# Kernel optimization log

Measured on AMD Instinct MI355X. Metric: run time of the kernel, lower is better.

Reference implementation:

```python
import jax, jax.numpy as jnp
import numpy as np

KER = 8

def _gelu(x):
    return jax.nn.gelu(x, approximate=False)

def _conv3x3(x, w, b):
    y = jax.lax.conv_general_dilated(x, w, (1, 1), 'SAME',
                                     dimension_numbers=('NCHW', 'OIHW', 'NCHW'))
    return y + b[None, :, None, None]

def _unfold(x):
    # F.unfold(kernel=8, stride=8): [B,C,H,W] -> [B, C*64, L], C-major then kh,kw
    B, C, H, W = x.shape
    Hb, Wb = H // KER, W // KER
    p = x.reshape(B, C, Hb, KER, Wb, KER).transpose(0, 1, 3, 5, 2, 4)
    return p.reshape(B, C * KER * KER, Hb * Wb)

def _fold(cols, H, W):
    # inverse of _unfold (non-overlapping patches)
    B, CK, L = cols.shape
    C = CK // (KER * KER)
    Hb, Wb = H // KER, W // KER
    p = cols.reshape(B, C, KER, KER, Hb, Wb).transpose(0, 1, 4, 2, 5, 3)
    return p.reshape(B, C, H, W)

def _bn(x, g, b, eps=1e-5):
    # train-mode BatchNorm1d on [B, C, L]: stats over (B, L) per channel
    m = x.mean(axis=(0, 2), keepdims=True)
    v = x.var(axis=(0, 2), keepdims=True)
    return (x - m) * jax.lax.rsqrt(v + eps) * g[None, :, None] + b[None, :, None]


def setup_inputs() -> dict:
    key = jax.random.key(0)
    ks = jax.random.split(key, 10)
    ind, d, hid = 64, 1024, 256
    f = lambda k, s: jax.random.normal(k, s, dtype=jnp.float32) * 0.02
    return {
        'feat': jax.random.normal(ks[0], (4, ind, 256, 256), dtype=jnp.float32),
        'w_enc': f(ks[1], (ind, ind, 3, 3)), 'b_enc': jnp.zeros((ind,), jnp.float32),
        'w_k': f(ks[2], (ind, ind, 3, 3)), 'b_k': jnp.zeros((ind,), jnp.float32),
        'w_v': f(ks[3], (ind, ind, 3, 3)), 'b_v': jnp.zeros((ind,), jnp.float32),
        'fcq_w': f(ks[4], (d, ind * KER * KER)), 'fcq_b': jnp.zeros((d,), jnp.float32),
        'fck_w': f(ks[5], (d, ind * KER * KER)), 'fck_b': jnp.zeros((d,), jnp.float32),
        'bnq_g': jnp.ones((d,), jnp.float32), 'bnq_b': jnp.zeros((d,), jnp.float32),
        'bnk_g': jnp.ones((d,), jnp.float32), 'bnk_b': jnp.zeros((d,), jnp.float32),
        'ff1_w': f(ks[6], (hid, ind)), 'ff1_b': jnp.zeros((hid,), jnp.float32),
        'ff2_w': f(ks[7], (ind, hid)), 'ff2_b': jnp.zeros((ind,), jnp.float32),
    }


def reference(feat, w_enc, b_enc, w_k, b_k, w_v, b_v,
              fcq_w, fcq_b, fck_w, fck_b, bnq_g, bnq_b, bnk_g, bnk_b,
              ff1_w, ff1_b, ff2_w, ff2_b):
    B, C, H, W = feat.shape
    fk = _gelu(_conv3x3(feat, w_k, b_k))
    fv = _gelu(_conv3x3(feat, w_v, b_v))
    refer = _gelu(_conv3x3(feat, w_enc, b_enc))
    q_un = _unfold(refer).transpose(0, 2, 1)   # [B, L, C*64]
    k_un = _unfold(fk).transpose(0, 2, 1)
    v_un = _unfold(fv).transpose(0, 2, 1)
    q = jnp.einsum('blc,dc->bld', q_un, fcq_w) + fcq_b
    q = _bn(q.transpose(0, 2, 1), bnq_g, bnq_b).transpose(0, 2, 1)  # [B, L, 1024]
    k = jnp.einsum('blc,dc->bld', k_un, fck_w) + fck_b
    k = _bn(k.transpose(0, 2, 1), bnk_g, bnk_b).transpose(0, 2, 1)
    scores = jnp.einsum('bld,bmd->blm', q, k) / jnp.sqrt(jnp.float32(q.shape[2]))
    attn = jax.nn.softmax(scores, axis=2)
    out = jnp.einsum('blm,bmc->blc', attn, v_un).transpose(0, 2, 1)  # [B, C*64, L]
    out = _fold(out, H, W)
    h = _gelu(jnp.einsum('bchw,oc->bohw', out, ff1_w) + ff1_b[None, :, None, None])
    h = _gelu(jnp.einsum('bchw,oc->bohw', h, ff2_w) + ff2_b[None, :, None, None])
    return h + feat
```

## Files before the change

kernel.cpp:

```cpp
#include <hip/hip_runtime.h>

typedef unsigned short u16;
typedef float f4 __attribute__((ext_vector_type(4)));
typedef float f32x4 __attribute__((ext_vector_type(4)));
typedef short bf16x8 __attribute__((ext_vector_type(8)));
typedef u16 u16x8 __attribute__((ext_vector_type(8)));
typedef u16 u16x4 __attribute__((ext_vector_type(4)));

__device__ __forceinline__ u16 f2bf(float f){
  unsigned u = __float_as_uint(f);
  u = (u + 0x7FFFu + ((u>>16)&1u)) >> 16;
  return (u16)u;
}
__device__ __forceinline__ float bf2f(u16 u){
  return __uint_as_float(((unsigned)u)<<16);
}
__device__ __forceinline__ float gelu_f(float x){
  float y = 1.5957691216057308f*(x + 0.044715f*x*x*x);
  y = fminf(y, 30.0f);
  float t = __expf(y);
  float r = __builtin_amdgcn_rcpf(t + 1.0f);
  return 0.5f*x*(1.0f + (t - 1.0f)*r);
}

typedef __attribute__((address_space(1))) const unsigned int as1_cuint;
typedef __attribute__((address_space(3))) unsigned int as3_uint;
__device__ __forceinline__ void gload_lds16(const void* g, void* l){
  __builtin_amdgcn_global_load_lds((as1_cuint*)g, (as3_uint*)l, 16, 0, 0);
}

__global__ __launch_bounds__(256) void to_nhwc(
    const float* __restrict__ F, u16* __restrict__ O)
{
  __shared__ float tile[64][65];
  const int t = threadIdx.x, b = blockIdx.y;
  const long px0 = (long)blockIdx.x*64;
  const float* Fb = F + (long)b*64*65536;
  #pragma unroll
  for (int i = 0; i < 4; ++i){
    const int ch = (t>>4) + i*16;
    const int pxo = (t&15)*4;
    f4 v = *(const f4*)&Fb[(long)ch*65536 + px0 + pxo];
    tile[ch][pxo]=v[0]; tile[ch][pxo+1]=v[1]; tile[ch][pxo+2]=v[2]; tile[ch][pxo+3]=v[3];
  }
  __syncthreads();
  const int px = t & 63, ch0 = (t>>6)*16;
  u16x8 o0, o1;
  #pragma unroll
  for (int j = 0; j < 8; ++j){ o0[j]=f2bf(tile[ch0+j][px]); o1[j]=f2bf(tile[ch0+8+j][px]); }
  u16* Ob = O + ((long)b*65536 + px0 + px)*64 + ch0;
  *(u16x8*)Ob = o0; *(u16x8*)(Ob+8) = o1;
}

__global__ __launch_bounds__(256) void wt_prep(
    const float* __restrict__ we, const float* __restrict__ wk,
    const float* __restrict__ wv, u16* __restrict__ Wt2)
{
  const int i = blockIdx.x*256 + threadIdx.x;
  const int cio = i & 31;
  const int t1 = i >> 5;
  const int n  = t1 % 192;
  const int t2 = t1 / 192;
  const int kc = t2 & 1, p = t2 >> 1;
  const int dy = p/3, dx = p - dy*3;
  const int ci = kc*32 + cio;
  const float* W = (n < 64) ? we : (n < 128) ? wk : wv;
  const int co = n & 63;
  Wt2[i] = f2bf(W[((co*64 + ci)*3 + dy)*3 + dx]);
}

__global__ __launch_bounds__(512,2) void conv_mfma(
    const u16* __restrict__ X, const u16* __restrict__ Wt2,
    const float* __restrict__ be, const float* __restrict__ bk, const float* __restrict__ bv,
    u16* __restrict__ Aq, u16* __restrict__ Ak, u16* __restrict__ Vl)
{
  __shared__ __align__(16) u16 smem[24576];
  const int t = threadIdx.x, lane = t & 63, wvi = t >> 6;
  const int bx = blockIdx.x, by = blockIdx.y, b = blockIdx.z;
  const int x0 = bx*16, y0 = by*8;
  const u16* Xb = X + (long)b*4194304;

  #pragma unroll
  for (int j = 0; j < 3; ++j){
    const int id = t + j*512;
    if (id < 1440){
      const int row = id / 144, rem = id - row*144, col = rem >> 3, ck = rem & 7;
      const int y = y0 - 1 + row, x = x0 - 1 + col;
      int4 v = {0,0,0,0};
      if ((unsigned)y < 256u && (unsigned)x < 256u)
        v = *(const int4*)(Xb + ((long)y*256 + x)*64 + ck*8);
      *(int4*)&smem[((row*18 + col)*8 + (ck ^ (col&7)))*8] = v;
    }
  }
  __syncthreads();

  const int wm4 = (wvi>>2)*4;
  const int wn  = (wvi&3)*48;
  const int fr = lane & 15, fo = lane >> 4;
  f32x4 acc[4][3] = {};

  #pragma unroll
  for (int dy = 0; dy < 3; ++dy)
  #pragma unroll
  for (int dx = 0; dx < 3; ++dx){
    const int p = dy*3 + dx;
    #pragma unroll
    for (int kc = 0; kc < 2; ++kc){
      bf16x8 af[4], bfv[3];
      const u16* wp = Wt2 + ((long)(p*2 + kc)*192 + wn + fr)*32 + fo*8;
      #pragma unroll
      for (int ni = 0; ni < 3; ++ni)
        bfv[ni] = *(const bf16x8*)(wp + ni*16*32);
      #pragma unroll
      for (int mi = 0; mi < 4; ++mi){
        const int row = wm4 + mi + dy;
        const int col = fr + dx;
        af[mi] = *(const bf16x8*)&smem[((row*18 + col)*8 + ((kc*4+fo) ^ (col&7)))*8];
      }
      #pragma unroll
      for (int mi = 0; mi < 4; ++mi)
        #pragma unroll
        for (int ni = 0; ni < 3; ++ni)
          acc[mi][ni] = __builtin_amdgcn_mfma_f32_16x16x32_bf16(af[mi], bfv[ni], acc[mi][ni], 0, 0, 0);
    }
  }
  __syncthreads();

  const int c0 = fo*4;
  const int lloc = c0 >> 3, kw0 = c0 & 7;
  #pragma unroll
  for (int ni = 0; ni < 3; ++ni){
    const int n = wn + ni*16 + fr;
    const int mat = n >> 6, co = n & 63;
    const float bias = (mat==0) ? be[co] : (mat==1) ? bk[co] : bv[co];
    #pragma unroll
    for (int mi = 0; mi < 4; ++mi){
      const int r = wm4 + mi;
      u16x4 o;
      #pragma unroll
      for (int rg = 0; rg < 4; ++rg) o[rg] = f2bf(gelu_f(acc[mi][ni][rg] + bias));
      const int e = ((mat*2 + lloc)*64 + co)*64 + ((r*8 + kw0) ^ ((co&7)<<3));
      *(u16x4*)&smem[e] = o;
    }
  }
  __syncthreads();

  const int l_lo = by*32 + bx*2;
  const int co_r = t >> 3, sw = (t&7) ^ (co_r&7);
  const int eoff = co_r*64 + sw*8;
  #pragma unroll
  for (int i = 0; i < 6; ++i){
    const int mat = i >> 1, ll = i & 1;
    u16x8 v = *(const u16x8*)&smem[(mat*2 + ll)*4096 + eoff];
    u16* dst = (mat==0 ? Aq : mat==1 ? Ak : Vl)
             + ((long)b*1024 + l_lo + ll)*4096 + t*8;
    *(u16x8*)dst = v;
  }
}

__global__ __launch_bounds__(256) void v_tr(
    const u16* __restrict__ S, u16* __restrict__ D)
{
  __shared__ u16 tl[64][72];
  const int t = threadIdx.x, b = blockIdx.z;
  const int ck0 = blockIdx.x*64, l0 = blockIdx.y*64;
  const u16* Sb = S + (long)b*4194304;
  u16* Db = D + (long)b*4194304;
  #pragma unroll
  for (int j = 0; j < 2; ++j){
    const int li = (t>>3) + j*32, cko = (t&7)*8;
    *(u16x8*)&tl[li][cko] = *(const u16x8*)(Sb + (long)(l0+li)*4096 + ck0 + cko);
  }
  __syncthreads();
  #pragma unroll
  for (int j = 0; j < 2; ++j){
    const int cki = (t>>3) + j*32, lo = (t&7)*8;
    u16x8 v;
    #pragma unroll
    for (int e = 0; e < 8; ++e) v[e] = tl[lo+e][cki];
    *(u16x8*)(Db + (long)(ck0+cki)*1024 + l0 + lo) = v;
  }
}

__device__ __forceinline__ void xcd_map(int gxl, int gyl, int n8l,
                                        int& bx, int& by, int& bz){
  const int s = blockIdx.x + (blockIdx.y<<gxl) + (blockIdx.z<<(gxl+gyl));
  const int orig = ((s & 7) << n8l) + (s >> 3);
  bx = orig & ((1<<gxl)-1);
  by = (orig >> gxl) & ((1<<gyl)-1);
  bz = orig >> (gxl+gyl);
}

template<int EPI>
__global__ __launch_bounds__(256,4) void gemm_bt64(
    const u16* __restrict__ A, long sA,
    const u16* __restrict__ B, long sB, const int zshB,
    void* __restrict__ Cv, long sC,
    const int M, const int N, const int K,
    float* __restrict__ bnstats,
    const int gxl, const int gyl, const int n8l)
{
  int bx, by, bI;
  xcd_map(gxl, gyl, n8l, bx, by, bI);
  const u16* Ab = A + (long)bI*sA;
  const u16* Bb = B + (long)(bI>>zshB)*sB;
  const int m0 = bx*64, n0 = by*128;
  __shared__ __align__(16) u16 As[4096];
  __shared__ __align__(16) u16 Bs[8192];
  const int t = threadIdx.x, lane = t & 63, wv = t >> 6;
  const int wm = (wv>>1)*32, wn = (wv&1)*64;
  const int fr = lane & 15, fo = lane >> 4;
  f32x4 acc[2][4] = {};
  const int ca  = wv*64 + lane;
  const int cb0 = wv*128 + lane, cb1 = cb0 + 64;
  const u16* Ag  = Ab + (long)(m0 + (ca >>2))*K + (ca &3)*8;
  const u16* Bg0 = Bb + (long)(n0 + (cb0>>2))*K + (cb0&3)*8;
  const u16* Bg1 = Bb + (long)(n0 + (cb1>>2))*K + (cb1&3)*8;
  gload_lds16(Ag,  &As[wv*512]);
  gload_lds16(Bg0, &Bs[wv*1024]);
  gload_lds16(Bg1, &Bs[wv*1024 + 512]);
  const int nk = K >> 5;
  int cur = 0;
  for (int ki = 0; ki < nk; ++ki){
    __syncthreads();
    if (ki + 1 < nk){
      const int k0 = (ki + 1) << 5;
      gload_lds16(Ag  + k0, &As[((cur^1)<<11) + wv*512]);
      gload_lds16(Bg0 + k0, &Bs[((cur^1)<<12) + wv*1024]);
      gload_lds16(Bg1 + k0, &Bs[((cur^1)<<12) + wv*1024 + 512]);
    }
    const int ra = cur << 11, rb = cur << 12;
    bf16x8 af[2], bfv[4];
    #pragma unroll
    for (int i = 0; i < 2; ++i)
      af[i]  = *(const bf16x8*)&As[ra + (wm + i*16 + fr)*32 + fo*8];
    #pragma unroll
    for (int i = 0; i < 4; ++i)
      bfv[i] = *(const bf16x8*)&Bs[rb + (wn + i*16 + fr)*32 + fo*8];
    #pragma unroll
    for (int mi = 0; mi < 2; ++mi)
      #pragma unroll
      for (int ni = 0; ni < 4; ++ni)
        acc[mi][ni] = __builtin_amdgcn_mfma_f32_16x16x32_bf16(af[mi], bfv[ni], acc[mi][ni], 0, 0, 0);
    cur ^= 1;
  }
  if (EPI == 0){
    float* Cf = (float*)Cv + (long)bI*sC;
    #pragma unroll
    for (int mi = 0; mi < 2; ++mi)
      #pragma unroll
      for (int ni = 0; ni < 4; ++ni){
        const int col = n0 + wn + ni*16 + fr;
        #pragma unroll
        for (int r = 0; r < 4; ++r){
          const int row = m0 + wm + mi*16 + fo*4 + r;
          Cf[(long)row*N + col] = acc[mi][ni][r];
        }
      }
  } else {
    u16* Cb = (u16*)Cv + (long)bI*sC;
    #pragma unroll
    for (int mi = 0; mi < 2; ++mi)
      #pragma unroll
      for (int ni = 0; ni < 4; ++ni){
        const int col = n0 + wn + ni*16 + fr;
        const int row0 = m0 + wm + mi*16 + fo*4;
        u16x4 o;
        #pragma unroll
        for (int r = 0; r < 4; ++r) o[r] = f2bf(acc[mi][ni][r]);
        *(u16x4*)&Cb[(long)col*M + row0] = o;
      }
    const int sel = bI >> 2;
    float* sums = bnstats + sel*2048;
    #pragma unroll
    for (int ni = 0; ni < 4; ++ni){
      float s = 0.f, q = 0.f;
      #pragma unroll
      for (int mi = 0; mi < 2; ++mi)
        #pragma unroll
        for (int r = 0; r < 4; ++r){
          const float v = acc[mi][ni][r];
          s += v; q += v*v;
        }
      s += __shfl_xor(s, 16); s += __shfl_xor(s, 32);
      q += __shfl_xor(q, 16); q += __shfl_xor(q, 32);
      if (fo == 0){
        const int col = n0 + wn + ni*16 + fr;
        atomicAdd(&sums[col], s);
        atomicAdd(&sums[1024 + col], q);
      }
    }
  }
}

__global__ __launch_bounds__(256,3) void gemm_bt(
    const u16* __restrict__ A, long sA,
    const u16* __restrict__ B, long sB,
    void* __restrict__ Cv,
    const int M, const int N, const int K,
    const int gxl, const int gyl, const int n8l)
{
  int bx, by, bI;
  xcd_map(gxl, gyl, n8l, bx, by, bI);
  const u16* Ab = A + (long)bI*sA;
  const u16* Bb = B + (long)bI*sB;
  const int m0 = bx*128, n0 = by*128;
  __shared__ __align__(16) u16 As[8192];
  __shared__ __align__(16) u16 Bs[8192];
  const int t = threadIdx.x, lane = t & 63, wv = t >> 6;
  const int wm = (wv>>1)*64, wn = (wv&1)*64;
  const int fr = lane & 15, fo = lane >> 4;
  f32x4 acc[4][4] = {};
  const int c0 = wv*128 + lane, c1 = c0 + 64;
  const u16* Ag0 = Ab + (long)(m0 + (c0>>2))*K + (c0&3)*8;
  const u16* Ag1 = Ab + (long)(m0 + (c1>>2))*K + (c1&3)*8;
  const u16* Bg0 = Bb + (long)(n0 + (c0>>2))*K + (c0&3)*8;
  const u16* Bg1 = Bb + (long)(n0 + (c1>>2))*K + (c1&3)*8;
  const int lo0 = wv*1024;
  gload_lds16(Ag0, &As[lo0]);
  gload_lds16(Ag1, &As[lo0 + 512]);
  gload_lds16(Bg0, &Bs[lo0]);
  gload_lds16(Bg1, &Bs[lo0 + 512]);
  const int nk = K >> 5;
  int cur = 0;
  for (int ki = 0; ki < nk; ++ki){
    __syncthreads();
    if (ki + 1 < nk){
      const int k0 = (ki + 1) << 5;
      const int so = ((cur^1) << 12) + lo0;
      gload_lds16(Ag0 + k0, &As[so]);
      gload_lds16(Ag1 + k0, &As[so + 512]);
      gload_lds16(Bg0 + k0, &Bs[so]);
      gload_lds16(Bg1 + k0, &Bs[so + 512]);
    }
    const int ro = cur << 12;
    bf16x8 af[4], bfv[4];
    #pragma unroll
    for (int i = 0; i < 4; ++i){
      af[i]  = *(const bf16x8*)&As[ro + (wm + i*16 + fr)*32 + fo*8];
      bfv[i] = *(const bf16x8*)&Bs[ro + (wn + i*16 + fr)*32 + fo*8];
    }
    #pragma unroll
    for (int mi = 0; mi < 4; ++mi)
      #pragma unroll
      for (int ni = 0; ni < 4; ++ni)
        acc[mi][ni] = __builtin_amdgcn_mfma_f32_16x16x32_bf16(af[mi], bfv[ni], acc[mi][ni], 0, 0, 0);
    cur ^= 1;
  }
  u16* O = (u16*)Cv;
  #pragma unroll
  for (int mi = 0; mi < 4; ++mi)
    #pragma unroll
    for (int ni = 0; ni < 4; ++ni){
      const int col = n0 + wn + ni*16 + fr;
      const int c = col >> 6, khh = (col>>3)&7, kww = col&7;
      #pragma unroll
      for (int r = 0; r < 4; ++r){
        const int row = m0 + wm + mi*16 + fo*4 + r;
        const int hb = row >> 5, wbb = row & 31;
        O[(((long)bI*65536 + (hb*8+khh)*256 + wbb*8 + kww)<<6) + c] = f2bf(acc[mi][ni][r]);
      }
    }
}

__global__ __launch_bounds__(256,3) void ff1_mfma(
    const u16* __restrict__ X, const u16* __restrict__ W1b,
    const float* __restrict__ B1, u16* __restrict__ H1)
{
  const int t = threadIdx.x, lane = t & 63, wv = t >> 6;
  const long m0 = (long)blockIdx.x*128 + (wv>>1)*64;
  const int n0 = blockIdx.y*128 + (wv&1)*64;
  const int fr = lane & 15, fo = lane >> 4;
  f32x4 acc[4][4] = {};
  #pragma unroll
  for (int k0 = 0; k0 < 64; k0 += 32){
    bf16x8 af[4], bfv[4];
    #pragma unroll
    for (int i = 0; i < 4; ++i){
      af[i]  = *(const bf16x8*)(X   + (m0 + i*16 + fr)*64 + k0 + fo*8);
      bfv[i] = *(const bf16x8*)(W1b + (long)(n0 + i*16 + fr)*64 + k0 + fo*8);
    }
    #pragma unroll
    for (int mi = 0; mi < 4; ++mi)
      #pragma unroll
      for (int ni = 0; ni < 4; ++ni)
        acc[mi][ni] = __builtin_amdgcn_mfma_f32_16x16x32_bf16(af[mi], bfv[ni], acc[mi][ni], 0, 0, 0);
  }
  #pragma unroll
  for (int ni = 0; ni < 4; ++ni){
    const int col = n0 + ni*16 + fr;
    const float bc = B1[col];
    #pragma unroll
    for (int mi = 0; mi < 4; ++mi){
      const long row = m0 + mi*16 + fo*4;
      #pragma unroll
      for (int r = 0; r < 4; ++r)
        H1[(row + r)*256 + col] = f2bf(gelu_f(acc[mi][ni][r] + bc));
    }
  }
}

__global__ __launch_bounds__(256,3) void ff2_mfma(
    const u16* __restrict__ H1, const u16* __restrict__ W2b,
    const float* __restrict__ B2, const float* __restrict__ F,
    float* __restrict__ OUT)
{
  const int t = threadIdx.x, lane = t & 63, wv = t >> 6;
  const long m0 = (long)blockIdx.x*256 + wv*64;
  const int fr = lane & 15, fo = lane >> 4;
  f32x4 acc[4][4] = {};
  for (int k0 = 0; k0 < 256; k0 += 32){
    bf16x8 af[4], bfv[4];
    #pragma unroll
    for (int i = 0; i < 4; ++i){
      af[i]  = *(const bf16x8*)(H1  + (m0 + i*16 + fr)*256 + k0 + fo*8);
      bfv[i] = *(const bf16x8*)(W2b + (long)(i*16 + fr)*256 + k0 + fo*8);
    }
    #pragma unroll
    for (int mi = 0; mi < 4; ++mi)
      #pragma unroll
      for (int ni = 0; ni < 4; ++ni)
        acc[mi][ni] = __builtin_amdgcn_mfma_f32_16x16x32_bf16(af[mi], bfv[ni], acc[mi][ni], 0, 0, 0);
  }
  #pragma unroll
  for (int ni = 0; ni < 4; ++ni){
    const int c = ni*16 + fr;
    const float bc = B2[c];
    #pragma unroll
    for (int mi = 0; mi < 4; ++mi){
      const long p = m0 + mi*16 + fo*4;
      const int b = (int)(p >> 16), pp = (int)(p & 65535);
      const long idx = ((long)(b*64 + c))*65536 + pp;
      const f4 fres = *(const f4*)&F[idx];
      f4 o;
      #pragma unroll
      for (int r = 0; r < 4; ++r) o[r] = gelu_f(acc[mi][ni][r] + bc) + fres[r];
      *(f4*)&OUT[idx] = o;
    }
  }
}

__global__ __launch_bounds__(256) void cvt_w(
    const float* __restrict__ Wq, const float* __restrict__ Wk,
    u16* __restrict__ Oq, u16* __restrict__ Ok)
{
  const long i = ((long)blockIdx.x*256 + threadIdx.x)*4;
  const float* s = blockIdx.y ? Wk : Wq;
  u16* d = blockIdx.y ? Ok : Oq;
  f4 v = *(const f4*)&s[i];
  u16x4 o; o[0]=f2bf(v[0]); o[1]=f2bf(v[1]); o[2]=f2bf(v[2]); o[3]=f2bf(v[3]);
  *(u16x4*)&d[i] = o;
}

__global__ __launch_bounds__(256) void cvt_ffw(
    const float* __restrict__ W1, const float* __restrict__ W2,
    u16* __restrict__ O1, u16* __restrict__ O2)
{
  const long i = ((long)blockIdx.x*256 + threadIdx.x)*4;
  const float* s = blockIdx.y ? W2 : W1;
  u16* d = blockIdx.y ? O2 : O1;
  f4 v = *(const f4*)&s[i];
  u16x4 o; o[0]=f2bf(v[0]); o[1]=f2bf(v[1]); o[2]=f2bf(v[2]); o[3]=f2bf(v[3]);
  *(u16x4*)&d[i] = o;
}

__global__ void bn_fin2(float* __restrict__ stats,
                        const float* __restrict__ gq, const float* __restrict__ bq,
                        const float* __restrict__ gk, const float* __restrict__ bk)
{
  const int sel = blockIdx.y;
  const int d = blockIdx.x*256 + threadIdx.x;
  if (d >= 1024) return;
  const float* sum   = stats + sel*2048;
  const float* sumsq = sum + 1024;
  const float* g    = sel ? gk : gq;
  const float* beta = sel ? bk : bq;
  const float m  = sum[d]   * (1.f/4096.f);
  const float vv = sumsq[d] * (1.f/4096.f) - m*m;
  const float sc = g[d] * rsqrtf(vv + 1e-5f);
  stats[4096 + sel*2048 + d]        = sc;
  stats[4096 + sel*2048 + 1024 + d] = beta[d] - m*sc;
}

__global__ __launch_bounds__(256) void bn_apply_t(
    const u16* __restrict__ QT, const float* __restrict__ stats,
    u16* __restrict__ Y)
{
  __shared__ u16 tl[64][72];
  const int t = threadIdx.x, zi = blockIdx.z;
  const int d0 = blockIdx.x*64, l0 = blockIdx.y*64;
  const int sel = zi >> 2;
  const u16* S = QT + (long)zi*1048576;
  u16* D = Y + (long)zi*1048576;
  const float* scp = stats + 4096 + sel*2048;
  const float* shp = scp + 1024;
  #pragma unroll
  for (int j = 0; j < 2; ++j){
    const int di = (t>>3) + j*32, lo = (t&7)*8;
    const int d = d0 + di;
    const float sc = scp[d], sh = shp[d];
    u16x8 v = *(const u16x8*)(S + (long)d*1024 + l0 + lo);
    u16x8 o;
    #pragma unroll
    for (int e = 0; e < 8; ++e) o[e] = f2bf(bf2f(v[e])*sc + sh);
    *(u16x8*)&tl[di][lo] = o;
  }
  __syncthreads();
  #pragma unroll
  for (int j = 0; j < 2; ++j){
    const int li = (t>>3) + j*32, dof = (t&7)*8;
    u16x8 v;
    #pragma unroll
    for (int e = 0; e < 8; ++e) v[e] = tl[dof+e][li];
    *(u16x8*)(D + (long)(l0+li)*1024 + d0 + dof) = v;
  }
}

__global__ __launch_bounds__(256) void softmax_k(
    const float* __restrict__ S, u16* __restrict__ P)
{
  const long row = blockIdx.x;
  const float* p = S + row*1024;
  const int t = threadIdx.x;
  f4 v = *(const f4*)&p[t*4];
  v *= 0.03125f;
  float mx = fmaxf(fmaxf(v[0],v[1]), fmaxf(v[2],v[3]));
  #pragma unroll
  for (int o = 1; o < 64; o <<= 1) mx = fmaxf(mx, __shfl_xor(mx, o));
  __shared__ float red[4], red2[4];
  if ((t & 63) == 0) red[t>>6] = mx;
  __syncthreads();
  mx = fmaxf(fmaxf(red[0],red[1]), fmaxf(red[2],red[3]));
  f4 e;
  e[0]=__expf(v[0]-mx); e[1]=__expf(v[1]-mx); e[2]=__expf(v[2]-mx); e[3]=__expf(v[3]-mx);
  float sm = e[0]+e[1]+e[2]+e[3];
  #pragma unroll
  for (int o = 1; o < 64; o <<= 1) sm += __shfl_xor(sm, o);
  if ((t & 63) == 0) red2[t>>6] = sm;
  __syncthreads();
  sm = red2[0]+red2[1]+red2[2]+red2[3];
  const float inv = 1.0f/sm;
  u16x4 o4; o4[0]=f2bf(e[0]*inv); o4[1]=f2bf(e[1]*inv); o4[2]=f2bf(e[2]*inv); o4[3]=f2bf(e[3]*inv);
  *(u16x4*)&P[row*1024 + t*4] = o4;
}

extern "C" void kernel_launch(void* const* d_in, const int* in_sizes, int n_in,
                              void* d_out, int out_size, void* d_ws, size_t ws_size,
                              hipStream_t stream)
{
  const float* feat  = (const float*)d_in[0];
  const float* w_enc = (const float*)d_in[1];
  const float* b_enc = (const float*)d_in[2];
  const float* w_k   = (const float*)d_in[3];
  const float* b_k   = (const float*)d_in[4];
  const float* w_v   = (const float*)d_in[5];
  const float* b_v   = (const float*)d_in[6];
  const float* fcq_w = (const float*)d_in[7];
  const float* fck_w = (const float*)d_in[9];
  const float* bnq_g = (const float*)d_in[11];
  const float* bnq_b = (const float*)d_in[12];
  const float* bnk_g = (const float*)d_in[13];
  const float* bnk_b = (const float*)d_in[14];
  const float* ff1w  = (const float*)d_in[15];
  const float* ff1b  = (const float*)d_in[16];
  const float* ff2w  = (const float*)d_in[17];
  const float* ff2b  = (const float*)d_in[18];

  char* ws = (char*)d_ws;
  u16*   Aq      = (u16*)  (ws);
  u16*   Ak      = (u16*)  (ws + (32ull<<20));
  u16*   Vc      = (u16*)  (ws + (64ull<<20));
  u16*   Wq      = (u16*)  (ws + (96ull<<20));
  u16*   Wk      = (u16*)  (ws + (104ull<<20));
  u16*   q_bf    = (u16*)  (ws + (112ull<<20));
  u16*   k_bf    = (u16*)  (ws + (120ull<<20));
  u16*   qk_rawT = (u16*)  (ws + (128ull<<20));
  float* scores  = (float*)(ws + (160ull<<20));
  u16*   attn    = (u16*)  (ws + (176ull<<20));
  u16*   out_nhwc= (u16*)  (ws + (184ull<<20));
  u16*   NX      = (u16*)  (ws + (128ull<<20));
  u16*   Vl      = (u16*)  (ws + (160ull<<20));
  u16*   Wt2     = (u16*)  (ws + (216ull<<20));
  float* stats   = (float*)(ws + (217ull<<20));
  u16*   W1b     = (u16*)  (ws + (218ull<<20));
  u16*   W2b     = (u16*)  (ws + (218ull<<20) + 65536);
  u16*   h1      = (u16*)  (ws);

  hipMemsetAsync(stats, 0, 4096*sizeof(float), stream);

  to_nhwc<<<dim3(1024,4), 256, 0, stream>>>(feat, NX);
  wt_prep<<<dim3(432), 256, 0, stream>>>(w_enc, w_k, w_v, Wt2);
  conv_mfma<<<dim3(16,32,4), 512, 0, stream>>>(NX, Wt2, b_enc, b_k, b_v, Aq, Ak, Vl);
  v_tr<<<dim3(64,16,4), 256, 0, stream>>>(Vl, Vc);
  cvt_w<<<dim3(4096,2), 256, 0, stream>>>(fcq_w, fck_w, Wq, Wk);
  cvt_ffw<<<dim3(16,2), 256, 0, stream>>>(ff1w, ff2w, W1b, W2b);

  gemm_bt64<2><<<dim3(16,8,8), 256, 0, stream>>>(Aq, 4194304, Wq, 4194304, 2,
                                                 qk_rawT, 1048576, 1024, 1024, 4096, stats,
                                                 4, 3, 7);

  bn_fin2<<<dim3(4,2), 256, 0, stream>>>(stats, bnq_g, bnq_b, bnk_g, bnk_b);
  bn_apply_t<<<dim3(16,16,8), 256, 0, stream>>>(qk_rawT, stats, q_bf);

  gemm_bt64<0><<<dim3(16,8,4), 256, 0, stream>>>(q_bf, 1048576, k_bf, 1048576, 0,
                                                 scores, 1048576, 1024, 1024, 1024, nullptr,
                                                 4, 3, 6);
  softmax_k<<<dim3(4096), 256, 0, stream>>>(scores, attn);

  gemm_bt<<<dim3(8,32,4), 256, 0, stream>>>(attn, 1048576, Vc, 4194304,
                                            out_nhwc, 1024, 4096, 1024,
                                            3, 5, 7);

  ff1_mfma<<<dim3(2048,2), 256, 0, stream>>>(out_nhwc, W1b, ff1b, h1);
  ff2_mfma<<<dim3(1024), 256, 0, stream>>>(h1, W2b, ff2b, feat, (float*)d_out);
}
```

Measured before the change: 526.2 us.

## Triple-buffer GEMM LDS staging with XOR swizzle and raised MFMA priority

Both bf16 GEMM kernels move from double to triple buffering of shared-memory tiles. Each iteration waits with a partial vmcnt and a raw s_barrier, so loads two k-steps ahead stay in flight while the current tile is computed. The global source column is XOR-swizzled to match the fragment read offsets, which reduces LDS bank conflicts. The MFMA block also runs at raised wave priority. The cost is 50% more LDS per block, which may lower occupancy, and the hand-written waitcnt/barrier asm is fragile.

```diff
diff --git a/kernel.cpp b/kernel.cpp
--- a/kernel.cpp
+++ b/kernel.cpp
@@ -27,6 +27,11 @@
 typedef __attribute__((address_space(3))) unsigned int as3_uint;
 __device__ __forceinline__ void gload_lds16(const void* g, void* l){
   __builtin_amdgcn_global_load_lds((as1_cuint*)g, (as3_uint*)l, 16, 0, 0);
+}
+
+__device__ __forceinline__ int gswz(int c){
+  const int r = c >> 2;
+  return (((c & 3) ^ ((r & 3) ^ ((r >> 2) & 3))) * 8);
 }
 
 __global__ __launch_bounds__(256) void to_nhwc(
@@ -205,45 +210,51 @@
   const u16* Ab = A + (long)bI*sA;
   const u16* Bb = B + (long)(bI>>zshB)*sB;
   const int m0 = bx*64, n0 = by*128;
-  __shared__ __align__(16) u16 As[4096];
-  __shared__ __align__(16) u16 Bs[8192];
+  __shared__ __align__(16) u16 As[6144];
+  __shared__ __align__(16) u16 Bs[12288];
   const int t = threadIdx.x, lane = t & 63, wv = t >> 6;
   const int wm = (wv>>1)*32, wn = (wv&1)*64;
   const int fr = lane & 15, fo = lane >> 4;
+  const int fosw = (fo ^ ((fr & 3) ^ ((fr >> 2) & 3))) * 8;
   f32x4 acc[2][4] = {};
   const int ca  = wv*64 + lane;
   const int cb0 = wv*128 + lane, cb1 = cb0 + 64;
-  const u16* Ag  = Ab + (long)(m0 + (ca >>2))*K + (ca &3)*8;
-  const u16* Bg0 = Bb + (long)(n0 + (cb0>>2))*K + (cb0&3)*8;
-  const u16* Bg1 = Bb + (long)(n0 + (cb1>>2))*K + (cb1&3)*8;
-  gload_lds16(Ag,  &As[wv*512]);
-  gload_lds16(Bg0, &Bs[wv*1024]);
-  gload_lds16(Bg1, &Bs[wv*1024 + 512]);
+  const u16* Ag  = Ab + (long)(m0 + (ca >>2))*K + gswz(ca);
+  const u16* Bg0 = Bb + (long)(n0 + (cb0>>2))*K + gswz(cb0);
+  const u16* Bg1 = Bb + (long)(n0 + (cb1>>2))*K + gswz(cb1);
+#define STAGE64(slot, kofs) { \
+    gload_lds16(Ag  + (kofs), &As[(slot)*2048 + wv*512]); \
+    gload_lds16(Bg0 + (kofs), &Bs[(slot)*4096 + wv*1024]); \
+    gload_lds16(Bg1 + (kofs), &Bs[(slot)*4096 + wv*1024 + 512]); }
+  STAGE64(0, 0)
+  STAGE64(1, 32)
   const int nk = K >> 5;
-  int cur = 0;
+  int sl = 0;
   for (int ki = 0; ki < nk; ++ki){
-    __syncthreads();
-    if (ki + 1 < nk){
-      const int k0 = (ki + 1) << 5;
-      gload_lds16(Ag  + k0, &As[((cur^1)<<11) + wv*512]);
-      gload_lds16(Bg0 + k0, &Bs[((cur^1)<<12) + wv*1024]);
-      gload_lds16(Bg1 + k0, &Bs[((cur^1)<<12) + wv*1024 + 512]);
-    }
-    const int ra = cur << 11, rb = cur << 12;
+    if (ki + 1 < nk) asm volatile("s_waitcnt vmcnt(3)\n\ts_barrier" ::: "memory");
+    else             asm volatile("s_waitcnt vmcnt(0)\n\ts_barrier" ::: "memory");
+    if (ki + 2 < nk){
+      const int s2 = (sl >= 1) ? sl - 1 : sl + 2;
+      STAGE64(s2, (ki + 2) << 5)
+    }
+    const int ra = sl*2048, rb = sl*4096;
     bf16x8 af[2], bfv[4];
     #pragma unroll
     for (int i = 0; i < 2; ++i)
-      af[i]  = *(const bf16x8*)&As[ra + (wm + i*16 + fr)*32 + fo*8];
+      af[i]  = *(const bf16x8*)&As[ra + (wm + i*16 + fr)*32 + fosw];
     #pragma unroll
     for (int i = 0; i < 4; ++i)
-      bfv[i] = *(const bf16x8*)&Bs[rb + (wn + i*16 + fr)*32 + fo*8];
+      bfv[i] = *(const bf16x8*)&Bs[rb + (wn + i*16 + fr)*32 + fosw];
+    __builtin_amdgcn_s_setprio(1);
     #pragma unroll
     for (int mi = 0; mi < 2; ++mi)
       #pragma unroll
       for (int ni = 0; ni < 4; ++ni)
         acc[mi][ni] = __builtin_amdgcn_mfma_f32_16x16x32_bf16(af[mi], bfv[ni], acc[mi][ni], 0, 0, 0);
-    cur ^= 1;
-  }
+    __builtin_amdgcn_s_setprio(0);
+    sl = (sl + 1 == 3) ? 0 : sl + 1;
+  }
+#undef STAGE64
   if (EPI == 0){
     float* Cf = (float*)Cv + (long)bI*sC;
     #pragma unroll
@@ -305,48 +316,53 @@
   const u16* Ab = A + (long)bI*sA;
   const u16* Bb = B + (long)bI*sB;
   const int m0 = bx*128, n0 = by*128;
-  __shared__ __align__(16) u16 As[8192];
-  __shared__ __align__(16) u16 Bs[8192];
+  __shared__ __align__(16) u16 As[12288];
+  __shared__ __align__(16) u16 Bs[12288];
   const int t = threadIdx.x, lane = t & 63, wv = t >> 6;
   const int wm = (wv>>1)*64, wn = (wv&1)*64;
   const int fr = lane & 15, fo = lane >> 4;
+  const int fosw = (fo ^ ((fr & 3) ^ ((fr >> 2) & 3))) * 8;
   f32x4 acc[4][4] = {};
   const int c0 = wv*128 + lane, c1 = c0 + 64;
-  const u16* Ag0 = Ab + (long)(m0 + (c0>>2))*K + (c0&3)*8;
-  const u16* Ag1 = Ab + (long)(m0 + (c1>>2))*K + (c1&3)*8;
-  const u16* Bg0 = Bb + (long)(n0 + (c0>>2))*K + (c0&3)*8;
-  const u16* Bg1 = Bb + (long)(n0 + (c1>>2))*K + (c1&3)*8;
-  const int lo0 = wv*1024;
-  gload_lds16(Ag0, &As[lo0]);
-  gload_lds16(Ag1, &As[lo0 + 512]);
-  gload_lds16(Bg0, &Bs[lo0]);
-  gload_lds16(Bg1, &Bs[lo0 + 512]);
+  const u16* Ag0 = Ab + (long)(m0 + (c0>>2))*K + gswz(c0);
+  const u16* Ag1 = Ab + (long)(m0 + (c1>>2))*K + gswz(c1);
+  const u16* Bg0 = Bb + (long)(n0 + (c0>>2))*K + gswz(c0);
+  const u16* Bg1 = Bb + (long)(n0 + (c1>>2))*K + gswz(c1);
+#define STAGE128(slot, kofs) { \
+    u16* a_ = &As[(slot)*4096 + wv*1024]; \
+    u16* b_ = &Bs[(slot)*4096 + wv*1024]; \
+    gload_lds16(Ag0 + (kofs), a_); \
+    gload_lds16(Ag1 + (kofs), a_ + 512); \
+    gload_lds16(Bg0 + (kofs), b_); \
+    gload_lds16(Bg1 + (kofs), b_ + 512); }
+  STAGE128(0, 0)
+  STAGE128(1, 32)
   const int nk = K >> 5;
-  int cur = 0;
+  int sl = 0;
   for (int ki = 0; ki < nk; ++ki){
-    __syncthreads();
-    if (ki + 1 < nk){
-      const int k0 = (ki + 1) << 5;
-      const int so = ((cur^1) << 12) + lo0;
-      gload_lds16(Ag0 + k0, &As[so]);
-      gload_lds16(Ag1 + k0, &As[so + 512]);
-      gload_lds16(Bg0 + k0, &Bs[so]);
-      gload_lds16(Bg1 + k0, &Bs[so + 512]);
-    }
-    const int ro = cur << 12;
+    if (ki + 1 < nk) asm volatile("s_waitcnt vmcnt(4)\n\ts_barrier" ::: "memory");
+    else             asm volatile("s_waitcnt vmcnt(0)\n\ts_barrier" ::: "memory");
+    if (ki + 2 < nk){
+      const int s2 = (sl >= 1) ? sl - 1 : sl + 2;
+      STAGE128(s2, (ki + 2) << 5)
+    }
+    const int ro = sl*4096;
     bf16x8 af[4], bfv[4];
     #pragma unroll
     for (int i = 0; i < 4; ++i){
-      af[i]  = *(const bf16x8*)&As[ro + (wm + i*16 + fr)*32 + fo*8];
-      bfv[i] = *(const bf16x8*)&Bs[ro + (wn + i*16 + fr)*32 + fo*8];
-    }
+      af[i]  = *(const bf16x8*)&As[ro + (wm + i*16 + fr)*32 + fosw];
+      bfv[i] = *(const bf16x8*)&Bs[ro + (wn + i*16 + fr)*32 + fosw];
+    }
+    __builtin_amdgcn_s_setprio(1);
     #pragma unroll
     for (int mi = 0; mi < 4; ++mi)
       #pragma unroll
       for (int ni = 0; ni < 4; ++ni)
         acc[mi][ni] = __builtin_amdgcn_mfma_f32_16x16x32_bf16(af[mi], bfv[ni], acc[mi][ni], 0, 0, 0);
-    cur ^= 1;
-  }
+    __builtin_amdgcn_s_setprio(0);
+    sl = (sl + 1 == 3) ? 0 : sl + 1;
+  }
+#undef STAGE128
   u16* O = (u16*)Cv;
   #pragma unroll
   for (int mi = 0; mi < 4; ++mi)
```

After: 545.1 us. 1.04x slower.
